# Kernel tuning notes

Hardware: AMD Instinct MI355X
Metric: run time of the kernel (lower is better)

The kernel has to match this reference:

```python
import jax, jax.numpy as jnp
import numpy as np

T, E = 16384, 1024   # frames, feature dim (WavLM-Large)
M, K = 8, 512        # number of kmeans models, clusters per model


def setup_inputs() -> dict:
    key = jax.random.key(0)
    k1, k2, k3 = jax.random.split(key, 3)
    emb = jax.random.normal(k1, (1, T, E), dtype=jnp.float32)
    centroids = jax.random.normal(k2, (M, K, E), dtype=jnp.float32)
    # per-frame random kmeans model choice (stride=1): replaces random.randint in the loop
    model_idx = jax.random.randint(k3, (T,), 0, M, dtype=jnp.int32)
    return {"emb": emb, "centroids": centroids, "model_idx": model_idx}


def reference(emb, centroids, model_idx):
    # emb: [1,T,E], centroids: [M,K,E], model_idx: [T] in [0,M)
    x = emb[0]  # [T,E]
    # squared euclidean distance from every frame to every centroid of every model
    # (argmin over squared dist == argmin over cdist)
    x_sq = jnp.sum(x * x, axis=-1)                      # [T]
    c_sq = jnp.sum(centroids * centroids, axis=-1)      # [M,K]
    dots = jnp.einsum('te,mke->tmk', x, centroids)      # [T,M,K]
    d_all = x_sq[:, None, None] - 2.0 * dots + c_sq[None, :, :]  # [T,M,K]
    # select the randomly chosen model's distances per frame
    d = jnp.take_along_axis(d_all, model_idx[:, None, None].astype(jnp.int32), axis=1)[:, 0, :]  # [T,K]
    codes = jnp.argmin(d, axis=-1)                      # [T]
    # embedding lookup: the quantizer's emb maps cluster id -> centroid vector
    out = centroids[model_idx, codes]                   # [T,E]
    return out[None]  # [1,T,E]
```

## Files before the change

### kernel.cpp

```cpp
#include <hip/hip_runtime.h>


#define T_FRAMES 16384
#define E_DIM    1024
#define M_MODELS 8
#define K_CLUST  512

#define FPB 32
#define NCH 8
#define ROWP 33

typedef __bf16 bf16x8 __attribute__((ext_vector_type(8)));
typedef float  floatx16 __attribute__((ext_vector_type(16)));

__device__ __forceinline__ bf16x8 cvt8(const float4 a, const float4 b) {
  bf16x8 h;
  h[0] = (__bf16)a.x; h[1] = (__bf16)a.y; h[2] = (__bf16)a.z; h[3] = (__bf16)a.w;
  h[4] = (__bf16)b.x; h[5] = (__bf16)b.y; h[6] = (__bf16)b.z; h[7] = (__bf16)b.w;
  return h;
}

__global__ __launch_bounds__(256) void k_cvt(const float* __restrict__ cent,
                                             float* __restrict__ out,
                                             double* __restrict__ csq64,
                                             const int* __restrict__ midx,
                                             int* __restrict__ hist) {
  const int b = blockIdx.x;
  const int m = b >> 6;
  const int cg = (b >> 2) & 15;
  const int q = b & 3;
  const int tid = threadIdx.x;
  const int row = tid >> 3;
  const int o = tid & 7;
  const int gk0 = q * 32 + o * 4;
  const int B32 = (m * 16 + cg) * 32;
  const float* src = cent + ((size_t)(m * K_CLUST + cg * 32 + row)) * E_DIM;
  double ss = 0.0;
#pragma unroll
  for (int j = 0; j < 4; ++j) {
    const int gk = gk0 + j;
    const float4 a = *(const float4*)(src + gk * 8);
    const float4 bb = *(const float4*)(src + gk * 8 + 4);
    ss += (double)a.x * a.x + (double)a.y * a.y + (double)a.z * a.z +
          (double)a.w * a.w + (double)bb.x * bb.x + (double)bb.y * bb.y +
          (double)bb.z * bb.z + (double)bb.w * bb.w;
    const size_t foff = (size_t)(B32 + (gk >> 2)) * 1024 + 512 +
                        ((gk & 3) * 32 + row) * 4;
    *(bf16x8*)(out + foff) = cvt8(a, bb);
  }
  __shared__ double csq_l[32][8];
  csq_l[row][o] = ss;
  __syncthreads();
  if (tid < 32) {
    double s = 0.0;
#pragma unroll
    for (int t = 0; t < 8; ++t) s += csq_l[tid][t];
    atomicAdd(&csq64[m * K_CLUST + cg * 32 + tid], s);
  }
  if (b < 64) {
    __shared__ int h[M_MODELS * 33];
    for (int i = tid; i < M_MODELS * 33; i += 256) h[i] = 0;
    __syncthreads();
    const int mm = midx[b * 256 + tid];
    atomicAdd(&h[mm * 33 + (tid & 31)], 1);
    __syncthreads();
    if (tid < M_MODELS) {
      int s = 0;
      for (int j = 0; j < 32; ++j) s += h[tid * 33 + j];
      hist[b * M_MODELS + tid] = s;
    }
  }
}

__global__ __launch_bounds__(256) void k_scatter(const int* __restrict__ midx,
                                                 const int* __restrict__ hist,
                                                 int* __restrict__ order,
                                                 int* __restrict__ offs) {
  __shared__ int h2[64 * M_MODELS];
  __shared__ int cur[M_MODELS];
  const int tid = threadIdx.x;
  h2[tid] = hist[tid];
  h2[tid + 256] = hist[tid + 256];
  __syncthreads();
  if (tid < M_MODELS) {
    int tot_before = 0;
    for (int mp = 0; mp < tid; ++mp)
      for (int b = 0; b < 64; ++b) tot_before += h2[b * M_MODELS + mp];
    int prior = 0;
    for (int b = 0; b < (int)blockIdx.x; ++b) prior += h2[b * M_MODELS + tid];
    cur[tid] = tot_before + prior;
  }
  if (blockIdx.x == 0 && tid <= M_MODELS) {
    int o = 0;
    for (int mp = 0; mp < tid; ++mp)
      for (int b = 0; b < 64; ++b) o += h2[b * M_MODELS + mp];
    offs[tid] = o;
  }
  __syncthreads();
  const int f = blockIdx.x * 256 + tid;
  const int pos = atomicAdd(&cur[midx[f]], 1);
  order[pos] = f;
}

__global__ __launch_bounds__(512, 2) void k_dist(const float* __restrict__ emb,
                                                 const float* __restrict__ cent,
                                                 const double* __restrict__ csq64,
                                                 const int* __restrict__ order,
                                                 const int* __restrict__ offs,
                                                 float* __restrict__ out) {
  const int m = blockIdx.x;
  const int o0 = offs[m];
  const int cnt = offs[m + 1] - o0;
  const int start = blockIdx.y * FPB;
  if (start >= cnt) return;
  const int nvalid = min(FPB, cnt - start);

  __shared__ __align__(16) __bf16 A_l[2 * 16 * ROWP * 8];
  __shared__ int rows_l[FPB];
  __shared__ float wmin_s[8][FPB];
  __shared__ int wcol_s[8][FPB];
  __shared__ float gmin_s[FPB];
  __shared__ int cnt_s[FPB];
  __shared__ int cand_s[FPB][32];

  const int tid = threadIdx.x;
  const int l = tid & 63;
  const int w = tid >> 6;
  const int ln = l & 31;
  const int lh = l >> 5;

  if (tid < FPB) rows_l[tid] = order[o0 + start + min(tid, nvalid - 1)];
  __syncthreads();

  const int s_row = tid >> 4;
  const int s_o = tid & 15;
  const float4* emb4 = (const float4*)emb;
  const size_t arow4 = (size_t)rows_l[s_row] * (E_DIM / 4);

  float4 pa[2];
  pa[0] = emb4[arow4 + s_o * 2 + 0];
  pa[1] = emb4[arow4 + s_o * 2 + 1];
  *(bf16x8*)(A_l + ((s_o)*ROWP + s_row) * 8) = cvt8(pa[0], pa[1]);

  const char* bbase[2];
#pragma unroll
  for (int ct = 0; ct < 2; ++ct) {
    const int cg = w * 2 + ct;
    bbase[ct] = (const char*)out + (size_t)(m * 16 + cg) * 131072 + 2048 + l * 16;
  }
#define LOADB(ct, kb) (*(const bf16x8*)(bbase[ct] + (((kb) >> 1) << 12) + (((kb) & 1) << 10)))

  bf16x8 bR[8][2];
#pragma unroll
  for (int d = 0; d < 8; ++d)
#pragma unroll
    for (int ct = 0; ct < 2; ++ct) bR[d][ct] = LOADB(ct, d);

  floatx16 acc[2] = {};

  for (int c = 0; c < NCH; ++c) {
    __syncthreads();
    const int buf = (c & 1) * 16;
    if (c + 1 < NCH) {
      pa[0] = emb4[arow4 + (c + 1) * 32 + s_o * 2 + 0];
      pa[1] = emb4[arow4 + (c + 1) * 32 + s_o * 2 + 1];
    }
#pragma unroll
    for (int jj = 0; jj < 8; ++jj) {
      const int kb = c * 8 + jj;
      const int p = kb & 7;
      const bf16x8 a0 = *(const bf16x8*)(A_l + ((buf + jj * 2 + lh) * ROWP + ln) * 8);
      acc[0] = __builtin_amdgcn_mfma_f32_32x32x16_bf16(a0, bR[p][0], acc[0], 0, 0, 0);
      acc[1] = __builtin_amdgcn_mfma_f32_32x32x16_bf16(a0, bR[p][1], acc[1], 0, 0, 0);
      if (kb + 8 < 64) {
        bR[p][0] = LOADB(0, kb + 8);
        bR[p][1] = LOADB(1, kb + 8);
      }
    }
    if (c + 1 < NCH) {
      const int nbuf = ((c + 1) & 1) * 16;
      *(bf16x8*)(A_l + ((nbuf + s_o) * ROWP + s_row) * 8) = cvt8(pa[0], pa[1]);
    }
  }
#undef LOADB

  float cs[2];
#pragma unroll
  for (int ct = 0; ct < 2; ++ct)
    cs[ct] = (float)csq64[m * K_CLUST + w * 64 + ct * 32 + ln];

#pragma unroll
  for (int r = 0; r < 16; ++r) {
    const int fr = (r & 3) + 8 * (r >> 2) + 4 * lh;
    float bm = cs[0] - 2.0f * acc[0][r];
    int bc = w * 64 + ln;
    {
      const float s = cs[1] - 2.0f * acc[1][r];
      if (s < bm) { bm = s; bc = w * 64 + 32 + ln; }
    }
#pragma unroll
    for (int sh = 1; sh <= 16; sh <<= 1) {
      const float om = __shfl_xor(bm, sh, 64);
      const int oc = __shfl_xor(bc, sh, 64);
      if (om < bm || (om == bm && oc < bc)) { bm = om; bc = oc; }
    }
    if (ln == 0) { wmin_s[w][fr] = bm; wcol_s[w][fr] = bc; }
  }
  __syncthreads();

  if (tid < FPB) {
    float g = wmin_s[0][tid];
    int gc = wcol_s[0][tid];
#pragma unroll
    for (int w2 = 1; w2 < 8; ++w2) {
      const float v = wmin_s[w2][tid];
      const int vc = wcol_s[w2][tid];
      if (v < g || (v == g && vc < gc)) { g = v; gc = vc; }
    }
    gmin_s[tid] = g;
    cnt_s[tid] = 0;
  }
  __syncthreads();

#pragma unroll
  for (int r = 0; r < 16; ++r) {
    const int fr = (r & 3) + 8 * (r >> 2) + 4 * lh;
    const float thr = gmin_s[fr] + 3.0f;
#pragma unroll
    for (int ct = 0; ct < 2; ++ct) {
      const float s = cs[ct] - 2.0f * acc[ct][r];
      if (s < thr) {
        const int ix = atomicAdd(&cnt_s[fr], 1);
        if (ix < 32) cand_s[fr][ix] = w * 64 + ct * 32 + ln;
      }
    }
  }
  __syncthreads();

  for (int i = 0; i < 4; ++i) {
    const int f = w * 4 + i;
    const int t = rows_l[f];
    const int n = min(cnt_s[f], 32);
    int code;
    if (n == 1) {
      code = cand_s[f][0];
    } else {
      float4 xv[4];
#pragma unroll
      for (int q = 0; q < 4; ++q)
        xv[q] = *(const float4*)(emb + (size_t)t * E_DIM + (q * 64 + l) * 4);
      double bd = 1e300;
      int bi = 1 << 30;
      for (int j = 0; j < n; ++j) {
        const int cc = cand_s[f][j];
        const float4* crow4 = (const float4*)(cent + ((size_t)(m * K_CLUST + cc)) * E_DIM);
        double s = 0.0;
#pragma unroll
        for (int q = 0; q < 4; ++q) {
          const float4 cv = crow4[q * 64 + l];
          s += (double)xv[q].x * cv.x + (double)xv[q].y * cv.y +
               (double)xv[q].z * cv.z + (double)xv[q].w * cv.w;
        }
#pragma unroll
        for (int sh = 32; sh >= 1; sh >>= 1) s += __shfl_xor(s, sh, 64);
        const double d = csq64[m * K_CLUST + cc] - 2.0 * s;
        if (d < bd || (d == bd && cc < bi)) { bd = d; bi = cc; }
      }
      code = bi;
    }
    if (t >= 4096) {
      const float4* crow = (const float4*)(cent + ((size_t)(m * K_CLUST + code)) * E_DIM);
      float4* drow = (float4*)(out + (size_t)t * E_DIM);
#pragma unroll
      for (int q = 0; q < 4; ++q) drow[q * 64 + l] = crow[q * 64 + l];
    } else if (l == 0) {
      *(int*)(out + (size_t)t * E_DIM) = code;
    }
  }
}

__global__ __launch_bounds__(256) void k_gather(const float* __restrict__ cent,
                                                const int* __restrict__ midx,
                                                float* __restrict__ out) {
  const int t = blockIdx.x * 4 + (threadIdx.x >> 6);
  const int l = threadIdx.x & 63;
  float* drow = out + (size_t)t * E_DIM;
  const int code = *(const int*)drow;
  const int m = midx[t];
  const float4* src = (const float4*)(cent + ((size_t)(m * K_CLUST + code)) * E_DIM);
  float4* dst = (float4*)drow;
#pragma unroll
  for (int q = 0; q < 4; ++q) dst[q * 64 + l] = src[q * 64 + l];
}

extern "C" void kernel_launch(void* const* d_in, const int* in_sizes, int n_in,
                              void* d_out, int out_size, void* d_ws, size_t ws_size,
                              hipStream_t stream) {
  const float* emb = (const float*)d_in[0];
  const float* cent = (const float*)d_in[1];
  const int* midx = (const int*)d_in[2];
  float* out = (float*)d_out;

  char* ws = (char*)d_ws;
  double* csq64 = (double*)(ws + 0);
  int* hist = (int*)(ws + 32768);
  int* offs = (int*)(ws + 34816);
  int* order = (int*)(ws + 34880);

  (void)hipMemsetAsync(csq64, 0, M_MODELS * K_CLUST * sizeof(double), stream);
  hipLaunchKernelGGL(k_cvt, dim3(512), dim3(256), 0, stream,
                     cent, out, csq64, midx, hist);
  hipLaunchKernelGGL(k_scatter, dim3(64), dim3(256), 0, stream, midx, hist, order, offs);
  hipLaunchKernelGGL(k_dist, dim3(M_MODELS, 80), dim3(512), 0, stream,
                     emb, cent, csq64, order, offs, out);
  hipLaunchKernelGGL(k_gather, dim3(4096 / 4), dim3(256), 0, stream,
                     cent, midx, out);
}
```

Before: 194.1 us.

## Load A operand directly from global into registers, dropping LDS staging

The frame-embedding operand is no longer staged through a double-buffered LDS tile with per-chunk block barriers. Each lane now loads its own fp32 row slice from global memory into a 4-deep register ring, converts it to bf16 on the fly, and feeds it straight to the MFMA. This removes the __syncthreads and LDS traffic in the main loop. In exchange, all 8 waves redundantly fetch the same A rows from global/L2, and the extra prefetch registers add pressure.

```diff
diff --git a/kernel.cpp b/kernel.cpp
--- a/kernel.cpp
+++ b/kernel.cpp
@@ -7,8 +7,6 @@
 #define K_CLUST  512
 
 #define FPB 32
-#define NCH 8
-#define ROWP 33
 
 typedef __bf16 bf16x8 __attribute__((ext_vector_type(8)));
 typedef float  floatx16 __attribute__((ext_vector_type(16)));
@@ -115,8 +113,6 @@
   if (start >= cnt) return;
   const int nvalid = min(FPB, cnt - start);
 
-  __shared__ __align__(16) __bf16 A_l[2 * 16 * ROWP * 8];
-  __shared__ int rows_l[FPB];
   __shared__ float wmin_s[8][FPB];
   __shared__ int wcol_s[8][FPB];
   __shared__ float gmin_s[FPB];
@@ -129,18 +125,9 @@
   const int ln = l & 31;
   const int lh = l >> 5;
 
-  if (tid < FPB) rows_l[tid] = order[o0 + start + min(tid, nvalid - 1)];
-  __syncthreads();
-
-  const int s_row = tid >> 4;
-  const int s_o = tid & 15;
+  const int myrow = order[o0 + start + min(ln, nvalid - 1)];
   const float4* emb4 = (const float4*)emb;
-  const size_t arow4 = (size_t)rows_l[s_row] * (E_DIM / 4);
-
-  float4 pa[2];
-  pa[0] = emb4[arow4 + s_o * 2 + 0];
-  pa[1] = emb4[arow4 + s_o * 2 + 1];
-  *(bf16x8*)(A_l + ((s_o)*ROWP + s_row) * 8) = cvt8(pa[0], pa[1]);
+  const size_t arow4 = (size_t)myrow * (E_DIM / 4) + lh * 2;
 
   const char* bbase[2];
 #pragma unroll
@@ -149,39 +136,36 @@
     bbase[ct] = (const char*)out + (size_t)(m * 16 + cg) * 131072 + 2048 + l * 16;
   }
 #define LOADB(ct, kb) (*(const bf16x8*)(bbase[ct] + (((kb) >> 1) << 12) + (((kb) & 1) << 10)))
-
+#define LOADA0(kb) (emb4[arow4 + (kb) * 4 + 0])
+#define LOADA1(kb) (emb4[arow4 + (kb) * 4 + 1])
+
+  float4 aR0[4], aR1[4];
   bf16x8 bR[8][2];
 #pragma unroll
-  for (int d = 0; d < 8; ++d)
-#pragma unroll
-    for (int ct = 0; ct < 2; ++ct) bR[d][ct] = LOADB(ct, d);
+  for (int d = 0; d < 4; ++d) { aR0[d] = LOADA0(d); aR1[d] = LOADA1(d); }
+#pragma unroll
+  for (int d = 0; d < 8; ++d) {
+    bR[d][0] = LOADB(0, d);
+    bR[d][1] = LOADB(1, d);
+  }
 
   floatx16 acc[2] = {};
 
-  for (int c = 0; c < NCH; ++c) {
-    __syncthreads();
-    const int buf = (c & 1) * 16;
-    if (c + 1 < NCH) {
-      pa[0] = emb4[arow4 + (c + 1) * 32 + s_o * 2 + 0];
-      pa[1] = emb4[arow4 + (c + 1) * 32 + s_o * 2 + 1];
-    }
-#pragma unroll
-    for (int jj = 0; jj < 8; ++jj) {
-      const int kb = c * 8 + jj;
-      const int p = kb & 7;
-      const bf16x8 a0 = *(const bf16x8*)(A_l + ((buf + jj * 2 + lh) * ROWP + ln) * 8);
-      acc[0] = __builtin_amdgcn_mfma_f32_32x32x16_bf16(a0, bR[p][0], acc[0], 0, 0, 0);
-      acc[1] = __builtin_amdgcn_mfma_f32_32x32x16_bf16(a0, bR[p][1], acc[1], 0, 0, 0);
-      if (kb + 8 < 64) {
-        bR[p][0] = LOADB(0, kb + 8);
-        bR[p][1] = LOADB(1, kb + 8);
-      }
-    }
-    if (c + 1 < NCH) {
-      const int nbuf = ((c + 1) & 1) * 16;
-      *(bf16x8*)(A_l + ((nbuf + s_o) * ROWP + s_row) * 8) = cvt8(pa[0], pa[1]);
-    }
-  }
+#pragma unroll
+  for (int kb = 0; kb < 64; ++kb) {
+    const int pa = kb & 3;
+    const int pb = kb & 7;
+    const bf16x8 a0 = cvt8(aR0[pa], aR1[pa]);
+    acc[0] = __builtin_amdgcn_mfma_f32_32x32x16_bf16(a0, bR[pb][0], acc[0], 0, 0, 0);
+    acc[1] = __builtin_amdgcn_mfma_f32_32x32x16_bf16(a0, bR[pb][1], acc[1], 0, 0, 0);
+    if (kb + 4 < 64) { aR0[pa] = LOADA0(kb + 4); aR1[pa] = LOADA1(kb + 4); }
+    if (kb + 8 < 64) {
+      bR[pb][0] = LOADB(0, kb + 8);
+      bR[pb][1] = LOADB(1, kb + 8);
+    }
+  }
+#undef LOADA0
+#undef LOADA1
 #undef LOADB
 
   float cs[2];
@@ -239,7 +223,7 @@
 
   for (int i = 0; i < 4; ++i) {
     const int f = w * 4 + i;
-    const int t = rows_l[f];
+    const int t = order[o0 + start + min(f, nvalid - 1)];
     const int n = min(cnt_s[f], 32);
     int code;
     if (n == 1) {
```

New measurement: 268.9 us. +38.5%, slower.
